# Kernel optimization log

Hardware: AMD Instinct MI355X
Metric: run time of the kernel (lower is better)

The kernel has to match this reference:

```python
import jax, jax.numpy as jnp
import numpy as np

KSIZE = 3
STRIDE = 1
PADDING = 1
DILATION = 1
C_IN = 16
C_OUT = 16


def setup_inputs() -> dict:
    key = jax.random.key(0)
    k1, k2, k3 = jax.random.split(key, 3)
    inputs = jax.random.normal(k1, (2, C_IN, 24, 24, 24, 24), dtype=jnp.float32)
    weight = jax.random.normal(k2, (C_OUT, C_IN * KSIZE ** 4), dtype=jnp.float32)
    bias = jax.random.normal(k3, (1, C_OUT, 1, 1, 1, 1), dtype=jnp.float32)
    return {"inputs": inputs, "weight": weight, "bias": bias}


def reference(inputs, weight, bias):
    # weight stored flattened: [C_out, C_in * k^4] -> [C_out, C_in, k, k, k, k]
    w = weight.reshape(C_OUT, C_IN, KSIZE, KSIZE, KSIZE, KSIZE)
    # General 4-spatial-dim convolution via XLA's ND conv.
    dn = jax.lax.ConvDimensionNumbers(
        lhs_spec=(0, 1, 2, 3, 4, 5),   # N, C, U, V, H, W
        rhs_spec=(0, 1, 2, 3, 4, 5),   # O, I, kU, kV, kH, kW
        out_spec=(0, 1, 2, 3, 4, 5),
    )
    out = jax.lax.conv_general_dilated(
        inputs, w,
        window_strides=(STRIDE,) * 4,
        padding=((PADDING, PADDING),) * 4,
        rhs_dilation=(DILATION,) * 4,
        dimension_numbers=dn,
    )
    return out + bias
```

## Files before the change

### kernel.cpp

```cpp
#include <hip/hip_runtime.h>

#define S 24
#define PLANE 576
#define CISTRIDE 331776
#define SLAB_B 21632
#define QSLAB_B 6656
#define QOFF 4992
#define A_BYTES 51200
#define WS_SLABS A_BYTES

typedef __attribute__((ext_vector_type(8))) short bf16x8;
typedef __attribute__((ext_vector_type(4))) float f32x4;

__device__ __forceinline__ ushort f2bf(float f) {
    unsigned int u = __builtin_bit_cast(unsigned int, f);
    unsigned int r = u + 0x7fffu + ((u >> 16) & 1u);
    return (ushort)(r >> 16);
}

__global__ void __launch_bounds__(256)
pack_in(const float* __restrict__ in, const float* __restrict__ wgt, char* __restrict__ ws) {
    __shared__ unsigned lds_t[16][288];

    const int b = blockIdx.x;
    const int nb = b / PLANE, uv = b % PLANE;
    const float* src = in + (size_t)nb * 16 * CISTRIDE + (size_t)uv * PLANE;
    char* dst = ws + WS_SLABS + (size_t)b * SLAB_B;
    const int t = threadIdx.x;

    float4 f[9];
    #pragma unroll
    for (int i = 0; i < 9; ++i) {
        int flat = i * 256 + t;
        int ci = flat / 144, q4 = flat % 144;
        f[i] = *(const float4*)(src + (size_t)ci * CISTRIDE + 4 * q4);
    }
    #pragma unroll
    for (int i = 0; i < 9; ++i) {
        int flat = i * 256 + t;
        int ci = flat / 144, q4 = flat % 144;
        uint2 pk;
        pk.x = (unsigned)f2bf(f[i].x) | ((unsigned)f2bf(f[i].y) << 16);
        pk.y = (unsigned)f2bf(f[i].z) | ((unsigned)f2bf(f[i].w) << 16);
        *(uint2*)&lds_t[ci][2 * q4] = pk;
    }
    __syncthreads();

    #pragma unroll
    for (int i = 0; i < 6; ++i) {
        int c = i * 256 + t;
        if (c < 1352) {
            int k = c >> 2;
            int row = k / 13;
            int pos2 = c ^ (row & 3);
            int pos = pos2 >> 1, h = pos2 & 1;
            int col = pos - row * 26;
            uint4 o = make_uint4(0, 0, 0, 0);
            if (row >= 1 && row <= 24 && col >= 1 && col <= 24) {
                int q = (row - 1) * 24 + (col - 1);
                int q2 = q >> 1, odd = q & 1;
                #pragma unroll
                for (int kk = 0; kk < 4; ++kk) {
                    unsigned a = lds_t[8 * h + 2 * kk][q2];
                    unsigned bb = lds_t[8 * h + 2 * kk + 1][q2];
                    unsigned val = odd ? ((a >> 16) | (bb & 0xffff0000u))
                                       : ((a & 0xffffu) | (bb << 16));
                    ((unsigned*)&o)[kk] = val;
                }
            }
            *(uint4*)(dst + (size_t)c * 16) = o;
        }
    }

    if (b == 0) {
        for (int i = t; i < 3200; i += 256) {
            int step = i >> 6;
            int tap = step / 5, s = step % 5;
            int lane = i & 63;
            int co = lane & 15, gA = lane >> 4;
            int o = 2 * s + (gA >> 1);
            int cib = (gA & 1) * 8;
            ushort vals[8];
            #pragma unroll
            for (int j = 0; j < 8; ++j) {
                int widx = co * 1296 + (cib + j) * 81 + tap * 9 + o;
                widx = widx < 20736 ? widx : 0;
                vals[j] = (tap <= 8 && o <= 8) ? f2bf(wgt[widx]) : (ushort)0;
            }
            uint4 pk;
            pk.x = vals[0] | ((unsigned)vals[1] << 16);
            pk.y = vals[2] | ((unsigned)vals[3] << 16);
            pk.z = vals[4] | ((unsigned)vals[5] << 16);
            pk.w = vals[6] | ((unsigned)vals[7] << 16);
            *(uint4*)(ws + (size_t)i * 16) = pk;
        }
    }
}

__global__ void __launch_bounds__(192, 4)
conv4d_main(const char* __restrict__ ws, const float* __restrict__ bias,
            float* __restrict__ out) {
    __shared__ __align__(16) char lds[2 * QSLAB_B];

    const int t = threadIdx.x, lane = t & 63, wvid = t >> 6;
    const int braw = blockIdx.x;
    const int b = (braw & 7) * 288 + (braw >> 3);
    const int nb = b / 1152, rem = b % 1152;
    const int u = rem / 48, rem2 = rem % 48;
    const int v0 = (rem2 >> 2) * 2, qq = rem2 & 3;

    const int n16 = lane & 15, g = lane >> 4;
    const int dh = n16 >> 3, dw = n16 & 7;
    const int half = g & 1, osel = g >> 1;

    int laneoff[2][5];
    #pragma unroll
    for (int trp = 0; trp < 2; ++trp)
        #pragma unroll
        for (int s = 0; s < 5; ++s) {
            int o = 2 * s + osel; if (o > 8) o = 8;
            int kh = o / 3, kw = o % 3;
            int r_off = dh + kh, c_off = dw + kw;
            int lin = (r_off * 26 + c_off) * 32 + half * 16;
            laneoff[trp][s] = lin ^ ((((trp << 1) + r_off) & 3) << 4);
        }

    f32x4 acc0[3], acc1[3];
    #pragma unroll
    for (int i = 0; i < 3; ++i) { acc0[i] = (f32x4){0,0,0,0}; acc1[i] = (f32x4){0,0,0,0}; }

    unsigned mask = 0;
    #pragma unroll
    for (int i = 0; i < 12; ++i) {
        int uu = u + (i >> 2) - 1, vv = v0 + (i & 3) - 1;
        if (uu >= 0 && uu < S && vv >= 0 && vv < S) mask |= 1u << i;
    }

    const char* slabs = ws + WS_SLABS;
    const int srcoff = qq * QOFF;
    #define SLAB_PTR(i_) (slabs + ((size_t)nb * PLANE + (u + ((i_) >> 2) - 1) * S + (v0 + ((i_) & 3) - 1)) * SLAB_B + srcoff)

    #define STAGE(bufsel_, src_) do {                                              \
        const char* _s = (src_);                                                   \
        _Pragma("unroll")                                                          \
        for (int r2 = 0; r2 < 3; ++r2) {                                           \
            int chunk = r2 * 192 + t;                                              \
            if (r2 < 2 || t < 32)                                                  \
                __builtin_amdgcn_global_load_lds(                                  \
                    (const __attribute__((address_space(1))) unsigned int*)(_s + (size_t)chunk * 16), \
                    (__attribute__((address_space(3))) unsigned int*)(lds + (bufsel_) * QSLAB_B + chunk * 16), \
                    16, 0, 0);                                                     \
        }                                                                          \
    } while (0)

    bf16x8 a0[5], a1[5];
    #define LOAD_A(tap_) do {                                                      \
        int _ku = (tap_) >> 2, _dv = ((tap_) & 3) - 1;                             \
        int _s0 = (_dv <= 1) ? (_ku * 3 + _dv + 1) : 9;                            \
        int _s1 = (_dv >= 0) ? (_ku * 3 + _dv) : 9;                                \
        const char* _ap0 = ws + (size_t)_s0 * 5120 + (size_t)lane * 16;            \
        const char* _ap1 = ws + (size_t)_s1 * 5120 + (size_t)lane * 16;            \
        _Pragma("unroll")                                                          \
        for (int s = 0; s < 5; ++s) {                                              \
            a0[s] = *(const bf16x8*)(_ap0 + s * 1024);                             \
            a1[s] = *(const bf16x8*)(_ap1 + s * 1024);                             \
        }                                                                          \
    } while (0)

    int cur = __ffs(mask) - 1;
    unsigned remm = mask >> (cur + 1);
    int nxt = remm ? (cur + 1 + __ffs(remm) - 1) : -1;

    STAGE(0, SLAB_PTR(cur));
    LOAD_A(cur);
    if (nxt >= 0) STAGE(1, SLAB_PTR(nxt));
    asm volatile("s_waitcnt vmcnt(10)" ::: "memory");
    __builtin_amdgcn_s_barrier();

    int cb = 0;
    while (1) {
        const char* bp = lds + cb * QSLAB_B + wvid * 256;
        #pragma unroll
        for (int tr = 0; tr < 3; ++tr) {
            const int trp = (tr + qq) & 1;
            const char* bpt = bp + tr * 1664;
            #pragma unroll
            for (int s = 0; s < 5; ++s) {
                bf16x8 bfr = *(const bf16x8*)(bpt + laneoff[trp][s]);
                acc0[tr] = __builtin_amdgcn_mfma_f32_16x16x32_bf16(a0[s], bfr, acc0[tr], 0, 0, 0);
                acc1[tr] = __builtin_amdgcn_mfma_f32_16x16x32_bf16(a1[s], bfr, acc1[tr], 0, 0, 0);
            }
        }
        if (nxt < 0) break;
        unsigned r2m = mask >> (nxt + 1);
        int nxt2 = r2m ? (nxt + 1 + __ffs(r2m) - 1) : -1;
        LOAD_A(nxt);
        asm volatile("s_waitcnt vmcnt(10)" ::: "memory");
        __builtin_amdgcn_s_barrier();
        if (nxt2 >= 0) STAGE(cb, SLAB_PTR(nxt2));
        cur = nxt; nxt = nxt2; cb ^= 1;
    }

    float bv[4];
    #pragma unroll
    for (int r = 0; r < 4; ++r) bv[r] = bias[g * 4 + r];
    float* outp0 = out + (size_t)nb * 16 * CISTRIDE + (size_t)(u * S + v0) * PLANE;
    float* outp1 = outp0 + PLANE;
    #pragma unroll
    for (int tr = 0; tr < 3; ++tr) {
        int row = qq * 6 + tr * 2 + dh;
        int col = wvid * 8 + dw;
        int pos = row * S + col;
        #pragma unroll
        for (int r = 0; r < 4; ++r) {
            outp0[(size_t)(g * 4 + r) * CISTRIDE + pos] = acc0[tr][r] + bv[r];
            outp1[(size_t)(g * 4 + r) * CISTRIDE + pos] = acc1[tr][r] + bv[r];
        }
    }
}

extern "C" void kernel_launch(void* const* d_in, const int* in_sizes, int n_in,
                              void* d_out, int out_size, void* d_ws, size_t ws_size,
                              hipStream_t stream) {
    const float* in   = (const float*)d_in[0];
    const float* wgt  = (const float*)d_in[1];
    const float* bias = (const float*)d_in[2];
    float* out        = (float*)d_out;
    char* ws          = (char*)d_ws;

    pack_in<<<dim3(1152), dim3(256), 0, stream>>>(in, wgt, ws);
    conv4d_main<<<dim3(2304), dim3(192), 0, stream>>>(ws, bias, out);
}
```

Measured before the change: 80.78 us.

## Read input slabs directly from global memory instead of LDS double-buffering

The main conv kernel stops staging input slabs into LDS with async global_load_lds and a double-buffered barrier pipeline. It now loads B fragments straight from global memory (served by cache) inside a simple loop over valid taps. The pack kernel drops the XOR swizzle, which existed only to avoid LDS bank conflicts, and gains a sched_barrier after the loads. This removes barriers and the LDS footprint, but loses explicit prefetch overlap, so every MFMA step now waits on global/L2 latency.

```diff
diff --git a/kernel.cpp b/kernel.cpp
--- a/kernel.cpp
+++ b/kernel.cpp
@@ -4,7 +4,6 @@
 #define PLANE 576
 #define CISTRIDE 331776
 #define SLAB_B 21632
-#define QSLAB_B 6656
 #define QOFF 4992
 #define A_BYTES 51200
 #define WS_SLABS A_BYTES
@@ -35,6 +34,8 @@
         int ci = flat / 144, q4 = flat % 144;
         f[i] = *(const float4*)(src + (size_t)ci * CISTRIDE + 4 * q4);
     }
+    __builtin_amdgcn_sched_barrier(0);
+
     #pragma unroll
     for (int i = 0; i < 9; ++i) {
         int flat = i * 256 + t;
@@ -50,11 +51,8 @@
     for (int i = 0; i < 6; ++i) {
         int c = i * 256 + t;
         if (c < 1352) {
-            int k = c >> 2;
-            int row = k / 13;
-            int pos2 = c ^ (row & 3);
-            int pos = pos2 >> 1, h = pos2 & 1;
-            int col = pos - row * 26;
+            int pos = c >> 1, h = c & 1;
+            int row = pos / 26, col = pos % 26;
             uint4 o = make_uint4(0, 0, 0, 0);
             if (row >= 1 && row <= 24 && col >= 1 && col <= 24) {
                 int q = (row - 1) * 24 + (col - 1);
@@ -100,8 +98,6 @@
 __global__ void __launch_bounds__(192, 4)
 conv4d_main(const char* __restrict__ ws, const float* __restrict__ bias,
             float* __restrict__ out) {
-    __shared__ __align__(16) char lds[2 * QSLAB_B];
-
     const int t = threadIdx.x, lane = t & 63, wvid = t >> 6;
     const int braw = blockIdx.x;
     const int b = (braw & 7) * 288 + (braw >> 3);
@@ -113,17 +109,14 @@
     const int dh = n16 >> 3, dw = n16 & 7;
     const int half = g & 1, osel = g >> 1;
 
-    int laneoff[2][5];
+    int laneoff[5];
     #pragma unroll
-    for (int trp = 0; trp < 2; ++trp)
-        #pragma unroll
-        for (int s = 0; s < 5; ++s) {
-            int o = 2 * s + osel; if (o > 8) o = 8;
-            int kh = o / 3, kw = o % 3;
-            int r_off = dh + kh, c_off = dw + kw;
-            int lin = (r_off * 26 + c_off) * 32 + half * 16;
-            laneoff[trp][s] = lin ^ ((((trp << 1) + r_off) & 3) << 4);
-        }
+    for (int s = 0; s < 5; ++s) {
+        int o = 2 * s + osel; if (o > 8) o = 8;
+        int kh = o / 3, kw = o % 3;
+        int r_off = dh + kh, c_off = dw + kw;
+        laneoff[s] = (r_off * 26 + wvid * 8 + c_off) * 32 + half * 16;
+    }
 
     f32x4 acc0[3], acc1[3];
     #pragma unroll
@@ -136,22 +129,7 @@
         if (uu >= 0 && uu < S && vv >= 0 && vv < S) mask |= 1u << i;
     }
 
-    const char* slabs = ws + WS_SLABS;
-    const int srcoff = qq * QOFF;
-    #define SLAB_PTR(i_) (slabs + ((size_t)nb * PLANE + (u + ((i_) >> 2) - 1) * S + (v0 + ((i_) & 3) - 1)) * SLAB_B + srcoff)
-
-    #define STAGE(bufsel_, src_) do {                                              \
-        const char* _s = (src_);                                                   \
-        _Pragma("unroll")                                                          \
-        for (int r2 = 0; r2 < 3; ++r2) {                                           \
-            int chunk = r2 * 192 + t;                                              \
-            if (r2 < 2 || t < 32)                                                  \
-                __builtin_amdgcn_global_load_lds(                                  \
-                    (const __attribute__((address_space(1))) unsigned int*)(_s + (size_t)chunk * 16), \
-                    (__attribute__((address_space(3))) unsigned int*)(lds + (bufsel_) * QSLAB_B + chunk * 16), \
-                    16, 0, 0);                                                     \
-        }                                                                          \
-    } while (0)
+    const char* slabs = ws + WS_SLABS + (size_t)qq * QOFF;
 
     bf16x8 a0[5], a1[5];
     #define LOAD_A(tap_) do {                                                      \
@@ -167,38 +145,21 @@
         }                                                                          \
     } while (0)
 
-    int cur = __ffs(mask) - 1;
-    unsigned remm = mask >> (cur + 1);
-    int nxt = remm ? (cur + 1 + __ffs(remm) - 1) : -1;
-
-    STAGE(0, SLAB_PTR(cur));
-    LOAD_A(cur);
-    if (nxt >= 0) STAGE(1, SLAB_PTR(nxt));
-    asm volatile("s_waitcnt vmcnt(10)" ::: "memory");
-    __builtin_amdgcn_s_barrier();
-
-    int cb = 0;
-    while (1) {
-        const char* bp = lds + cb * QSLAB_B + wvid * 256;
+    unsigned m = mask;
+    while (m) {
+        const int cur = __ffs(m) - 1; m &= m - 1;
+        LOAD_A(cur);
+        const char* base = slabs +
+            ((size_t)nb * PLANE + (u + (cur >> 2) - 1) * S + (v0 + (cur & 3) - 1)) * SLAB_B;
         #pragma unroll
         for (int tr = 0; tr < 3; ++tr) {
-            const int trp = (tr + qq) & 1;
-            const char* bpt = bp + tr * 1664;
             #pragma unroll
             for (int s = 0; s < 5; ++s) {
-                bf16x8 bfr = *(const bf16x8*)(bpt + laneoff[trp][s]);
+                bf16x8 bfr = *(const bf16x8*)(base + tr * 1664 + laneoff[s]);
                 acc0[tr] = __builtin_amdgcn_mfma_f32_16x16x32_bf16(a0[s], bfr, acc0[tr], 0, 0, 0);
                 acc1[tr] = __builtin_amdgcn_mfma_f32_16x16x32_bf16(a1[s], bfr, acc1[tr], 0, 0, 0);
             }
         }
-        if (nxt < 0) break;
-        unsigned r2m = mask >> (nxt + 1);
-        int nxt2 = r2m ? (nxt + 1 + __ffs(r2m) - 1) : -1;
-        LOAD_A(nxt);
-        asm volatile("s_waitcnt vmcnt(10)" ::: "memory");
-        __builtin_amdgcn_s_barrier();
-        if (nxt2 >= 0) STAGE(cb, SLAB_PTR(nxt2));
-        cur = nxt; nxt = nxt2; cb ^= 1;
     }
 
     float bv[4];
```

Result: slower. 105.5 us (+30.6%).
